# Optimization experiments

Hardware: AMD Instinct MI355X
Metric: run time of the kernel (lower is better)

## Reference

```python
import jax, jax.numpy as jnp
import numpy as np

BN_EPS = 1e-3
EPS = 1e-8
IGNORE = -1


def _head(x, w1, b1, g, be, w2, b2):
    # Linear -> BatchNorm1d (training: batch stats, biased var) -> ReLU -> Linear
    h = x @ w1 + b1
    mu = h.mean(axis=0)
    var = h.var(axis=0)  # biased, matches torch BN normalization
    h = (h - mu) * jax.lax.rsqrt(var + BN_EPS) * g + be
    h = jax.nn.relu(h)
    return h @ w2 + b2


def _bias_losses(a, b, mask):
    # faithful to compute_loss(bias_gt, bias_pred, mask); l1 and cosine are symmetric
    dist = jnp.sum(jnp.abs(a - b), axis=-1)
    denom = jnp.sum(mask) + EPS
    l1 = jnp.sum(dist * mask) / denom
    an = a / (jnp.linalg.norm(a, axis=-1, keepdims=True) + EPS)
    bn = b / (jnp.linalg.norm(b, axis=-1, keepdims=True) + EPS)
    cos = -jnp.sum(an * bn, axis=-1)
    cl = jnp.sum(cos * mask) / denom
    return l1, cl


def setup_inputs() -> dict:
    key = jax.random.key(0)
    ks = jax.random.split(key, 12)
    N, C, S = 1048576, 64, 20
    inp = {
        'feat': jax.random.normal(ks[0], (N, C), jnp.float32),
        'coord': jax.random.normal(ks[1], (N, 3), jnp.float32) * 2.0,
        'segment': jax.random.randint(ks[2], (N,), -1, S).astype(jnp.int32),
        'instance': jax.random.randint(ks[3], (N,), -1, 200).astype(jnp.int32),
        'instance_centroid': jax.random.normal(ks[4], (N, 3), jnp.float32) * 2.0,
        'w1_xy': jax.random.normal(ks[5], (C, C), jnp.float32) * 0.05,
        'b1_xy': jnp.zeros((C,), jnp.float32),
        'g_xy': jnp.ones((C,), jnp.float32),
        'be_xy': jnp.zeros((C,), jnp.float32),
        'w2_xy': jax.random.normal(ks[6], (C, 2), jnp.float32) * 0.05,
        'b2_xy': jnp.zeros((2,), jnp.float32),
        'w1_z': jax.random.normal(ks[7], (C, C), jnp.float32) * 0.05,
        'b1_z': jnp.zeros((C,), jnp.float32),
        'g_z': jnp.ones((C,), jnp.float32),
        'be_z': jnp.zeros((C,), jnp.float32),
        'w2_z': jax.random.normal(ks[8], (C, 1), jnp.float32) * 0.05,
        'b2_z': jnp.zeros((1,), jnp.float32),
        'w_seg': jax.random.normal(ks[9], (C, S), jnp.float32) * 0.05,
        'b_seg': jnp.zeros((S,), jnp.float32),
    }
    return inp


def reference(feat, coord, segment, instance, instance_centroid,
              w1_xy, b1_xy, g_xy, be_xy, w2_xy, b2_xy,
              w1_z, b1_z, g_z, be_z, w2_z, b2_z,
              w_seg, b_seg):
    bias_pred_xy = _head(feat, w1_xy, b1_xy, g_xy, be_xy, w2_xy, b2_xy)  # [N,2]
    bias_pred_z = _head(feat, w1_z, b1_z, g_z, be_z, w2_z, b2_z)         # [N,1]
    logit_pred = feat @ w_seg + b_seg                                     # [N,S]

    # cross-entropy with ignore_index=-1, unit class weights
    valid = (segment != IGNORE)
    tgt = jnp.where(valid, segment, 0)
    logp = jax.nn.log_softmax(logit_pred, axis=-1)
    nll = -jnp.take_along_axis(logp, tgt[:, None], axis=1)[:, 0]
    vf = valid.astype(logit_pred.dtype)
    seg_loss = jnp.sum(nll * vf) / jnp.sum(vf)

    mask = (instance != IGNORE).astype(feat.dtype)
    bias_gt = instance_centroid - coord
    l1_xy, cos_xy = _bias_losses(bias_gt[:, :2], bias_pred_xy, mask)
    l1_z, cos_z = _bias_losses(bias_gt[:, 2:3], bias_pred_z, mask)

    # faithful to original (bias_xy_l1 counted twice, xy cosine unused in total)
    loss = seg_loss + l1_xy + l1_xy + 0.5 * (l1_z + cos_z)
    return (loss, seg_loss, l1_xy, cos_xy, l1_z, cos_z)
```

## Files before the change

### kernel.cpp

```cpp
#include <hip/hip_runtime.h>
#include <hip/hip_bf16.h>

#define OFF_COLSUM 0
#define OFF_S      64
#define OFF_ACC    4160
#define OFF_DONE   4168
#define OFF_ZEND   4169
#define OFF_SHX    4176
#define OFF_SHZ    4240
#define OFF_W1XS   4304
#define OFF_W1ZS   6352
#define OFF_WSEGS  8400

typedef __attribute__((ext_vector_type(8))) short bf16x8;
typedef __attribute__((ext_vector_type(4))) float f32x4;

__device__ __forceinline__ unsigned short f2bfh(float x) {
    __hip_bfloat16 h = __float2bfloat16(x);
    return *reinterpret_cast<unsigned short*>(&h);
}

union BF8 { bf16x8 v; unsigned short u[8]; };

__device__ __forceinline__ void gload_lds16(const void* g, void* l) {
    __builtin_amdgcn_global_load_lds((const __attribute__((address_space(1))) void*)g,
                                     (__attribute__((address_space(3))) void*)l, 16, 0, 0);
}


__global__ __launch_bounds__(256, 2) void k_stats(const float* __restrict__ feat,
                                                  int N, int ntiles, int tpb,
                                                  float* __restrict__ ws) {
    __shared__ __align__(16) float ftile[2][4096];
    const int t = threadIdx.x;
    const int lane = t & 63, l15 = lane & 15, grp = lane >> 4, wv = t >> 6;

    const f32x4 z4 = {0.f, 0.f, 0.f, 0.f};
    f32x4 acc[4] = {z4, z4, z4, z4};
    float csum = 0.f;

    const int l3 = l15 & 3;
    const int cb_base = l15 >> 2;
    const int g1x8 = (grp & 1) * 8;

    const int ti0 = blockIdx.x * tpb;
    const int tiend = min(ti0 + tpb, ntiles);

    auto stage = [&](int bufi, int ti) {
        const int row0 = ti * 64;
        if (row0 + 64 <= N) {
#pragma unroll
            for (int c = 0; c < 4; c++) {
                const int r = (wv * 4 + c) * 4 + grp;
                const int u = l15 ^ (r & 15);
                gload_lds16(&feat[(size_t)(row0 + r) * 64 + u * 4],
                            &ftile[bufi][(wv * 4 + c) * 256]);
            }
        } else {
#pragma unroll
            for (int u2 = 0; u2 < 4; u2++) {
                const int i = t + u2 * 256;
                const int r = i >> 4, u = (i & 15) ^ (r & 15);
                float4 v = make_float4(0.f, 0.f, 0.f, 0.f);
                if (row0 + r < N) v = *(const float4*)&feat[(size_t)(row0 + r) * 64 + u * 4];
                *(float4*)&ftile[bufi][i * 4] = v;
            }
        }
    };

    if (ti0 < tiend) stage(0, ti0);
    int cur = 0;
    for (int ti = ti0; ti < tiend; ++ti) {
        __syncthreads();
        if (ti + 1 < tiend) stage(cur ^ 1, ti + 1);
        const float* fb = ftile[cur];

        bf16x8 fr[4][2];
#pragma unroll
        for (int s = 0; s < 4; s++) {
            const int g = (wv + s) & 3;
            const int cb = (g * 4 + cb_base) ^ g1x8;
#pragma unroll
            for (int h = 0; h < 2; h++) {
                const int pbase = h * 32 + grp * 8;
                float vs[8];
#pragma unroll
                for (int kk = 0; kk < 8; kk++)
                    vs[kk] = fb[(pbase + kk) * 64 + ((cb ^ kk) << 2) + l3];
                BF8 fv;
#pragma unroll
                for (int kk = 0; kk < 8; kk++) fv.u[kk] = f2bfh(vs[kk]);
                fr[s][h] = fv.v;
                if (s == 0) {
#pragma unroll
                    for (int kk = 0; kk < 8; kk++) csum += vs[kk];
                }
            }
        }
#pragma unroll
        for (int s = 0; s < 4; s++) {
            acc[s] = __builtin_amdgcn_mfma_f32_16x16x32_bf16(fr[0][0], fr[s][0], acc[s], 0, 0, 0);
            acc[s] = __builtin_amdgcn_mfma_f32_16x16x32_bf16(fr[0][1], fr[s][1], acc[s], 0, 0, 0);
        }
        cur ^= 1;
    }

    float* S = ws + OFF_S;
#pragma unroll
    for (int s = 0; s < 4; s++) {
        const int gj = (wv + s) & 3;
#pragma unroll
        for (int r = 0; r < 4; r++)
            atomicAdd(&S[(wv * 16 + grp * 4 + r) * 64 + gj * 16 + l15], acc[s][r]);
    }
    csum += __shfl_xor(csum, 16);
    csum += __shfl_xor(csum, 32);
    if (grp == 0) atomicAdd(&ws[OFF_COLSUM + wv * 16 + l15], csum);
}

__global__ __launch_bounds__(256) void k_prep(
    const float* __restrict__ w1xy, const float* __restrict__ b1xy,
    const float* __restrict__ gxy,  const float* __restrict__ bexy,
    const float* __restrict__ w1z,  const float* __restrict__ b1z,
    const float* __restrict__ gz,   const float* __restrict__ bez,
    const float* __restrict__ wseg, float Nf, float* __restrict__ ws) {
    __shared__ float S[64][64];
    __shared__ float cs[64];
    const int t = threadIdx.x;

    for (int i = t; i < 4096; i += 256) ((float*)S)[i] = ws[OFF_S + i];
    if (t < 64) cs[t] = ws[OFF_COLSUM + t];
    __syncthreads();

    if (t < 128) {
        const int head = t >> 6, j = t & 63;
        const float* w1 = head ? w1z : w1xy;
        float w[64];
#pragma unroll
        for (int k = 0; k < 64; k++) w[k] = w1[k * 64 + j];
        float d = 0.f;
#pragma unroll
        for (int k = 0; k < 64; k++) d = fmaf(cs[k], w[k], d);
        float quad = 0.f;
#pragma unroll
        for (int k = 0; k < 64; k++) {
            float rd = 0.f;
#pragma unroll
            for (int l = 0; l < 64; l++) rd = fmaf(S[k][l], w[l], rd);
            quad = fmaf(w[k], rd, quad);
        }
        const float b1 = head ? b1z[j] : b1xy[j];
        const float mu  = d / Nf + b1;
        const float eh2 = quad / Nf + 2.f * b1 * d / Nf + b1 * b1;
        const float var = eh2 - mu * mu;
        const float g  = head ? gz[j]  : gxy[j];
        const float be = head ? bez[j] : bexy[j];
        const float sc = g * rsqrtf(var + 1e-3f);
        const float sh = be - mu * sc;
        ws[(head ? OFF_SHZ : OFF_SHX) + j] = sh;
        unsigned short* dst = (unsigned short*)(ws + (head ? OFF_W1ZS : OFF_W1XS));
#pragma unroll
        for (int k = 0; k < 64; k++) dst[j * 64 + k] = f2bfh(w[k] * sc);
    } else if (t < 160) {
        const int j = t - 128;
        unsigned short* dst = (unsigned short*)(ws + OFF_WSEGS);
        for (int k = 0; k < 64; k++)
            dst[j * 64 + k] = (j < 20) ? f2bfh(wseg[k * 20 + j]) : (unsigned short)0;
    }
}

__global__ __launch_bounds__(256, 2) void k_loss(
    const float* __restrict__ feat, const float* __restrict__ coord,
    const int* __restrict__ seg, const int* __restrict__ inst,
    const float* __restrict__ cent,
    const unsigned short* __restrict__ w1xs, const unsigned short* __restrict__ w1zs,
    const unsigned short* __restrict__ wsegs,
    const float* __restrict__ shxv, const float* __restrict__ shzv,
    const float* __restrict__ w2xy, const float* __restrict__ b2xy,
    const float* __restrict__ w2z,  const float* __restrict__ b2z,
    const float* __restrict__ bseg,
    int N, int ntiles, int tpb, float* __restrict__ acc, float* __restrict__ out) {
    __shared__ __align__(16) float ftile[2][4096];
    __shared__ float red[4][8];

    const int t = threadIdx.x;
    const int lane = t & 63, l15 = lane & 15, grp = lane >> 4, wv = t >> 6;

    bf16x8 ax[4][2], az[4][2], ag[2][2];
#pragma unroll
    for (int nt = 0; nt < 4; nt++)
#pragma unroll
        for (int h = 0; h < 2; h++) {
            ax[nt][h] = *(const bf16x8*)&w1xs[(nt * 16 + l15) * 64 + grp * 8 + h * 32];
            az[nt][h] = *(const bf16x8*)&w1zs[(nt * 16 + l15) * 64 + grp * 8 + h * 32];
        }
#pragma unroll
    for (int nt = 0; nt < 2; nt++)
#pragma unroll
        for (int h = 0; h < 2; h++)
            ag[nt][h] = *(const bf16x8*)&wsegs[(nt * 16 + l15) * 64 + grp * 8 + h * 32];

    float shx_c[4][4], shz_c[4][4], w20[4][4], w21[4][4], w2zc[4][4], bs_c[2][4];
#pragma unroll
    for (int nt = 0; nt < 4; nt++)
#pragma unroll
        for (int r = 0; r < 4; r++) {
            const int c = nt * 16 + grp * 4 + r;
            shx_c[nt][r] = shxv[c]; shz_c[nt][r] = shzv[c];
            w20[nt][r] = w2xy[c * 2]; w21[nt][r] = w2xy[c * 2 + 1];
            w2zc[nt][r] = w2z[c];
        }
#pragma unroll
    for (int nt = 0; nt < 2; nt++)
#pragma unroll
        for (int r = 0; r < 4; r++) {
            const int c = nt * 16 + grp * 4 + r;
            bs_c[nt][r] = (c < 20) ? bseg[c] : -1e30f;
        }
    const float pb0 = b2xy[0], pb1 = b2xy[1], pbz = b2z[0];

    float s_nll = 0.f, s_vf = 0.f, s_l1xy = 0.f, s_cosxy = 0.f;
    float s_l1z = 0.f, s_cosz = 0.f, s_mask = 0.f;

    const int ti0 = blockIdx.x * tpb;
    const int tiend = min(ti0 + tpb, ntiles);

    auto stage = [&](int bufi, int ti) {
        const int row0 = ti * 64;
        if (row0 + 64 <= N) {
#pragma unroll
            for (int c = 0; c < 4; c++) {
                const int r = (wv * 4 + c) * 4 + grp;
                const int u = l15 ^ (r & 15);
                gload_lds16(&feat[(size_t)(row0 + r) * 64 + u * 4],
                            &ftile[bufi][(wv * 4 + c) * 256]);
            }
        } else {
#pragma unroll
            for (int u2 = 0; u2 < 4; u2++) {
                const int i = t + u2 * 256;
                const int r = i >> 4, u = (i & 15) ^ (r & 15);
                float4 v = make_float4(0.f, 0.f, 0.f, 0.f);
                if (row0 + r < N) v = *(const float4*)&feat[(size_t)(row0 + r) * 64 + u * 4];
                *(float4*)&ftile[bufi][i * 4] = v;
            }
        }
    };

    int p_tg = -1, p_iv = -1;
    float p_c0 = 0.f, p_c1 = 0.f, p_c2 = 0.f, p_e0 = 0.f, p_e1 = 0.f, p_e2 = 0.f;
    auto ptload = [&](int ti) {
        const int gp = ti * 64 + wv * 16 + l15;
        const bool inb = (gp < N);
        p_tg = inb ? seg[gp] : -1;
        p_iv = inb ? inst[gp] : -1;
        if (inb) {
            p_c0 = coord[(size_t)gp * 3]; p_c1 = coord[(size_t)gp * 3 + 1]; p_c2 = coord[(size_t)gp * 3 + 2];
            p_e0 = cent[(size_t)gp * 3];  p_e1 = cent[(size_t)gp * 3 + 1];  p_e2 = cent[(size_t)gp * 3 + 2];
        } else {
            p_c0 = p_c1 = p_c2 = p_e0 = p_e1 = p_e2 = 0.f;
        }
    };

    if (ti0 < tiend) { stage(0, ti0); ptload(ti0); }
    int cur = 0;
    for (int ti = ti0; ti < tiend; ++ti) {
        const int tg = p_tg, iv = p_iv;
        const float c0 = p_c0, c1 = p_c1, c2 = p_c2, e0 = p_e0, e1 = p_e1, e2 = p_e2;

        __syncthreads();
        if (ti + 1 < tiend) { stage(cur ^ 1, ti + 1); ptload(ti + 1); }

        const int p = wv * 16 + l15;
        const float* fb = ftile[cur];
        const float4 q0 = *(const float4*)&fb[(p * 16 + ((grp * 2)     ^ l15)) * 4];
        const float4 q1 = *(const float4*)&fb[(p * 16 + ((grp * 2 + 1) ^ l15)) * 4];
        const float4 q2 = *(const float4*)&fb[(p * 16 + ((8 + grp * 2) ^ l15)) * 4];
        const float4 q3 = *(const float4*)&fb[(p * 16 + ((9 + grp * 2) ^ l15)) * 4];
        BF8 b0, b1;
        b0.u[0] = f2bfh(q0.x); b0.u[1] = f2bfh(q0.y); b0.u[2] = f2bfh(q0.z); b0.u[3] = f2bfh(q0.w);
        b0.u[4] = f2bfh(q1.x); b0.u[5] = f2bfh(q1.y); b0.u[6] = f2bfh(q1.z); b0.u[7] = f2bfh(q1.w);
        b1.u[0] = f2bfh(q2.x); b1.u[1] = f2bfh(q2.y); b1.u[2] = f2bfh(q2.z); b1.u[3] = f2bfh(q2.w);
        b1.u[4] = f2bfh(q3.x); b1.u[5] = f2bfh(q3.y); b1.u[6] = f2bfh(q3.z); b1.u[7] = f2bfh(q3.w);

        f32x4 cg0 = {bs_c[0][0], bs_c[0][1], bs_c[0][2], bs_c[0][3]};
        cg0 = __builtin_amdgcn_mfma_f32_16x16x32_bf16(ag[0][0], b0.v, cg0, 0, 0, 0);
        cg0 = __builtin_amdgcn_mfma_f32_16x16x32_bf16(ag[0][1], b1.v, cg0, 0, 0, 0);
        f32x4 cg1 = {bs_c[1][0], bs_c[1][1], bs_c[1][2], bs_c[1][3]};
        cg1 = __builtin_amdgcn_mfma_f32_16x16x32_bf16(ag[1][0], b0.v, cg1, 0, 0, 0);
        cg1 = __builtin_amdgcn_mfma_f32_16x16x32_bf16(ag[1][1], b1.v, cg1, 0, 0, 0);
        float lmax = cg0[0];
#pragma unroll
        for (int r = 1; r < 4; r++) lmax = fmaxf(lmax, cg0[r]);
#pragma unroll
        for (int r = 0; r < 4; r++) lmax = fmaxf(lmax, cg1[r]);
        lmax = fmaxf(lmax, __shfl_xor(lmax, 16));
        lmax = fmaxf(lmax, __shfl_xor(lmax, 32));
        float se = 0.f;
#pragma unroll
        for (int r = 0; r < 4; r++) se += __expf(cg0[r] - lmax);
#pragma unroll
        for (int r = 0; r < 4; r++) se += __expf(cg1[r] - lmax);
        se += __shfl_xor(se, 16); se += __shfl_xor(se, 32);
        const float lse = lmax + __logf(se);
        float lt = 0.f;
#pragma unroll
        for (int r = 0; r < 4; r++) lt += (grp * 4 + r == tg) ? cg0[r] : 0.f;
#pragma unroll
        for (int r = 0; r < 4; r++) lt += (16 + grp * 4 + r == tg) ? cg1[r] : 0.f;
        lt += __shfl_xor(lt, 16); lt += __shfl_xor(lt, 32);
        const float vf = (tg >= 0) ? 1.f : 0.f;
        s_nll += (lse - lt) * vf;
        s_vf += vf;

        float s0 = 0.f, s1 = 0.f, szv = 0.f;
#pragma unroll
        for (int nt = 0; nt < 4; nt++) {
            f32x4 cc = {shx_c[nt][0], shx_c[nt][1], shx_c[nt][2], shx_c[nt][3]};
            cc = __builtin_amdgcn_mfma_f32_16x16x32_bf16(ax[nt][0], b0.v, cc, 0, 0, 0);
            cc = __builtin_amdgcn_mfma_f32_16x16x32_bf16(ax[nt][1], b1.v, cc, 0, 0, 0);
#pragma unroll
            for (int r = 0; r < 4; r++) {
                const float hx = fmaxf(cc[r], 0.f);
                s0 = fmaf(hx, w20[nt][r], s0);
                s1 = fmaf(hx, w21[nt][r], s1);
            }
            f32x4 cz = {shz_c[nt][0], shz_c[nt][1], shz_c[nt][2], shz_c[nt][3]};
            cz = __builtin_amdgcn_mfma_f32_16x16x32_bf16(az[nt][0], b0.v, cz, 0, 0, 0);
            cz = __builtin_amdgcn_mfma_f32_16x16x32_bf16(az[nt][1], b1.v, cz, 0, 0, 0);
#pragma unroll
            for (int r = 0; r < 4; r++) {
                const float hz = fmaxf(cz[r], 0.f);
                szv = fmaf(hz, w2zc[nt][r], szv);
            }
        }
        s0 += __shfl_xor(s0, 16);  s0 += __shfl_xor(s0, 32);
        s1 += __shfl_xor(s1, 16);  s1 += __shfl_xor(s1, 32);
        szv += __shfl_xor(szv, 16); szv += __shfl_xor(szv, 32);
        const float p0 = s0 + pb0, p1 = s1 + pb1, pz = szv + pbz;

        const float mk = (iv >= 0) ? 1.f : 0.f;
        const float a0 = e0 - c0, a1 = e1 - c1, a2 = e2 - c2;
        s_l1xy += (fabsf(a0 - p0) + fabsf(a1 - p1)) * mk;
        const float na = sqrtf(a0 * a0 + a1 * a1) + 1e-8f;
        const float nb = sqrtf(p0 * p0 + p1 * p1) + 1e-8f;
        s_cosxy -= ((a0 * p0 + a1 * p1) / (na * nb)) * mk;
        s_l1z += fabsf(a2 - pz) * mk;
        const float naz = fabsf(a2) + 1e-8f, nbz = fabsf(pz) + 1e-8f;
        s_cosz -= ((a2 * pz) / (naz * nbz)) * mk;
        s_mask += mk;

        cur ^= 1;
    }

    float v[7] = {s_nll * 0.25f, s_vf * 0.25f, s_l1xy * 0.25f, s_cosxy * 0.25f,
                  s_l1z * 0.25f, s_cosz * 0.25f, s_mask * 0.25f};
#pragma unroll
    for (int i = 0; i < 7; i++) {
#pragma unroll
        for (int o = 32; o > 0; o >>= 1) v[i] += __shfl_down(v[i], o);
    }
    if (lane == 0) {
#pragma unroll
        for (int i = 0; i < 7; i++) red[wv][i] = v[i];
    }
    __syncthreads();
    if (t < 7) {
        float s = red[0][t] + red[1][t] + red[2][t] + red[3][t];
        atomicAdd(&acc[t], s);
    }
    __syncthreads();
    if (t == 0) {
        __threadfence();
        int* done = (int*)(acc + (OFF_DONE - OFF_ACC));
        if (atomicAdd(done, 1) == (int)gridDim.x - 1) {
            __threadfence();
            float sv[7];
#pragma unroll
            for (int i = 0; i < 7; i++) sv[i] = atomicAdd(&acc[i], 0.f);
            const float segl = sv[0] / sv[1];
            const float den = sv[6] + 1e-8f;
            const float l1xy = sv[2] / den, cosxy = sv[3] / den;
            const float l1z = sv[4] / den, cosz = sv[5] / den;
            out[0] = segl + l1xy + l1xy + 0.5f * (l1z + cosz);
            out[1] = segl;
            out[2] = l1xy;
            out[3] = cosxy;
            out[4] = l1z;
            out[5] = cosz;
        }
    }
}

extern "C" void kernel_launch(void* const* d_in, const int* in_sizes, int n_in,
                              void* d_out, int out_size, void* d_ws, size_t ws_size,
                              hipStream_t stream) {
    const float* feat  = (const float*)d_in[0];
    const float* coord = (const float*)d_in[1];
    const int*   segm  = (const int*)d_in[2];
    const int*   inst  = (const int*)d_in[3];
    const float* cent  = (const float*)d_in[4];
    const float* w1xy  = (const float*)d_in[5];
    const float* b1xy  = (const float*)d_in[6];
    const float* gxy   = (const float*)d_in[7];
    const float* bexy  = (const float*)d_in[8];
    const float* w2xy  = (const float*)d_in[9];
    const float* b2xy  = (const float*)d_in[10];
    const float* w1z   = (const float*)d_in[11];
    const float* b1z   = (const float*)d_in[12];
    const float* gz    = (const float*)d_in[13];
    const float* bez   = (const float*)d_in[14];
    const float* w2z   = (const float*)d_in[15];
    const float* b2z   = (const float*)d_in[16];
    const float* wseg  = (const float*)d_in[17];
    const float* bseg  = (const float*)d_in[18];

    const int N = in_sizes[0] / 64;
    float* ws = (float*)d_ws;
    const int ntiles = (N + 63) >> 6;

    const int grid_s = 512;
    const int tpb_s = (ntiles + grid_s - 1) / grid_s;
    const int grid_l = 512;
    const int tpb_l = (ntiles + grid_l - 1) / grid_l;

    hipMemsetAsync(d_ws, 0, OFF_ZEND * sizeof(float), stream);

    k_stats<<<grid_s, 256, 0, stream>>>(feat, N, ntiles, tpb_s, ws);
    k_prep<<<1, 256, 0, stream>>>(w1xy, b1xy, gxy, bexy, w1z, b1z, gz, bez, wseg,
                                  (float)N, ws);
    k_loss<<<grid_l, 256, 0, stream>>>(
        feat, coord, segm, inst, cent,
        (const unsigned short*)(ws + OFF_W1XS),
        (const unsigned short*)(ws + OFF_W1ZS),
        (const unsigned short*)(ws + OFF_WSEGS),
        ws + OFF_SHX, ws + OFF_SHZ,
        w2xy, b2xy, w2z, b2z, bseg, N, ntiles, tpb_l,
        ws + OFF_ACC, (float*)d_out);
}
```

Baseline: 188.9 us.

## Stage feat tile via registers as transposed bf16 in LDS for stats GEMM

The Gram/column-sum kernel now loads feat rows into registers, converts them to bf16 once, and writes a transposed, swizzled, packed bf16 tile to LDS. The MFMA fragments then come from single 16-byte LDS reads instead of eight scalar fp32 reads plus conversions per fragment. This replaces async global_load_lds double buffering with register prefetch and a single LDS buffer that needs two barriers per tile. It cuts LDS traffic and conversion work, at the cost of less overlap between memory and compute and more register pressure.

```diff
diff --git a/kernel.cpp b/kernel.cpp
--- a/kernel.cpp
+++ b/kernel.cpp
@@ -27,82 +27,81 @@
                                      (__attribute__((address_space(3))) void*)l, 16, 0, 0);
 }
 
-
 __global__ __launch_bounds__(256, 2) void k_stats(const float* __restrict__ feat,
                                                   int N, int ntiles, int tpb,
                                                   float* __restrict__ ws) {
-    __shared__ __align__(16) float ftile[2][4096];
+    __shared__ __align__(16) unsigned int bt[64 * 36];
     const int t = threadIdx.x;
     const int lane = t & 63, l15 = lane & 15, grp = lane >> 4, wv = t >> 6;
+    const int q = t & 15;
+    const int pp = t >> 4;
 
     const f32x4 z4 = {0.f, 0.f, 0.f, 0.f};
     f32x4 acc[4] = {z4, z4, z4, z4};
-    float csum = 0.f;
-
-    const int l3 = l15 & 3;
-    const int cb_base = l15 >> 2;
-    const int g1x8 = (grp & 1) * 8;
+    float cs4[4] = {0.f, 0.f, 0.f, 0.f};
+
+    const int sw_w = 4 * (q & 7);
+    int woff[4][2];
+#pragma unroll
+    for (int c = 0; c < 4; c++) {
+        woff[c][0] = (4 * q + c) * 36 + (pp ^ sw_w);
+        woff[c][1] = (4 * q + c) * 36 + ((pp + 16) ^ sw_w);
+    }
+    int roff[4][2];
+#pragma unroll
+    for (int s = 0; s < 4; s++) {
+        const int g = (wv + s) & 3;
+        const int ch = g * 16 + l15;
+        const int sw = 4 * ((ch >> 2) & 7);
+#pragma unroll
+        for (int h = 0; h < 2; h++)
+            roff[s][h] = ch * 72 + 2 * ((h * 16 + grp * 4) ^ sw);
+    }
 
     const int ti0 = blockIdx.x * tpb;
     const int tiend = min(ti0 + tpb, ntiles);
 
-    auto stage = [&](int bufi, int ti) {
-        const int row0 = ti * 64;
-        if (row0 + 64 <= N) {
-#pragma unroll
-            for (int c = 0; c < 4; c++) {
-                const int r = (wv * 4 + c) * 4 + grp;
-                const int u = l15 ^ (r & 15);
-                gload_lds16(&feat[(size_t)(row0 + r) * 64 + u * 4],
-                            &ftile[bufi][(wv * 4 + c) * 256]);
-            }
-        } else {
-#pragma unroll
-            for (int u2 = 0; u2 < 4; u2++) {
-                const int i = t + u2 * 256;
-                const int r = i >> 4, u = (i & 15) ^ (r & 15);
-                float4 v = make_float4(0.f, 0.f, 0.f, 0.f);
-                if (row0 + r < N) v = *(const float4*)&feat[(size_t)(row0 + r) * 64 + u * 4];
-                *(float4*)&ftile[bufi][i * 4] = v;
-            }
-        }
+    float4 fA0, fA1, fB0, fB1;
+    auto gload = [&](int ti) {
+        const int p0 = ti * 64 + 2 * pp;
+        const int pB = p0 + 32;
+        fA0 = make_float4(0.f, 0.f, 0.f, 0.f); fA1 = fA0; fB0 = fA0; fB1 = fA0;
+        if (p0 < N)     fA0 = *(const float4*)&feat[(size_t)p0 * 64 + q * 4];
+        if (p0 + 1 < N) fA1 = *(const float4*)&feat[(size_t)(p0 + 1) * 64 + q * 4];
+        if (pB < N)     fB0 = *(const float4*)&feat[(size_t)pB * 64 + q * 4];
+        if (pB + 1 < N) fB1 = *(const float4*)&feat[(size_t)(pB + 1) * 64 + q * 4];
     };
-
-    if (ti0 < tiend) stage(0, ti0);
-    int cur = 0;
+    auto commit = [&]() {
+        const float a0[4] = {fA0.x, fA0.y, fA0.z, fA0.w};
+        const float a1[4] = {fA1.x, fA1.y, fA1.z, fA1.w};
+        const float b0[4] = {fB0.x, fB0.y, fB0.z, fB0.w};
+        const float b1[4] = {fB1.x, fB1.y, fB1.z, fB1.w};
+#pragma unroll
+        for (int c = 0; c < 4; c++) {
+            cs4[c] += a0[c] + a1[c] + b0[c] + b1[c];
+            bt[woff[c][0]] = (unsigned)f2bfh(a0[c]) | ((unsigned)f2bfh(a1[c]) << 16);
+            bt[woff[c][1]] = (unsigned)f2bfh(b0[c]) | ((unsigned)f2bfh(b1[c]) << 16);
+        }
+    };
+
+    if (ti0 < tiend) gload(ti0);
     for (int ti = ti0; ti < tiend; ++ti) {
+        commit();
         __syncthreads();
-        if (ti + 1 < tiend) stage(cur ^ 1, ti + 1);
-        const float* fb = ftile[cur];
-
+        if (ti + 1 < tiend) gload(ti + 1);
+        const unsigned short* bu = (const unsigned short*)bt;
         bf16x8 fr[4][2];
 #pragma unroll
-        for (int s = 0; s < 4; s++) {
-            const int g = (wv + s) & 3;
-            const int cb = (g * 4 + cb_base) ^ g1x8;
-#pragma unroll
-            for (int h = 0; h < 2; h++) {
-                const int pbase = h * 32 + grp * 8;
-                float vs[8];
-#pragma unroll
-                for (int kk = 0; kk < 8; kk++)
-                    vs[kk] = fb[(pbase + kk) * 64 + ((cb ^ kk) << 2) + l3];
-                BF8 fv;
-#pragma unroll
-                for (int kk = 0; kk < 8; kk++) fv.u[kk] = f2bfh(vs[kk]);
-                fr[s][h] = fv.v;
-                if (s == 0) {
-#pragma unroll
-                    for (int kk = 0; kk < 8; kk++) csum += vs[kk];
-                }
-            }
-        }
+        for (int s = 0; s < 4; s++)
+#pragma unroll
+            for (int h = 0; h < 2; h++)
+                fr[s][h] = *(const bf16x8*)&bu[roff[s][h]];
 #pragma unroll
         for (int s = 0; s < 4; s++) {
             acc[s] = __builtin_amdgcn_mfma_f32_16x16x32_bf16(fr[0][0], fr[s][0], acc[s], 0, 0, 0);
             acc[s] = __builtin_amdgcn_mfma_f32_16x16x32_bf16(fr[0][1], fr[s][1], acc[s], 0, 0, 0);
         }
-        cur ^= 1;
+        __syncthreads();
     }
 
     float* S = ws + OFF_S;
@@ -113,9 +112,12 @@
         for (int r = 0; r < 4; r++)
             atomicAdd(&S[(wv * 16 + grp * 4 + r) * 64 + gj * 16 + l15], acc[s][r]);
     }
-    csum += __shfl_xor(csum, 16);
-    csum += __shfl_xor(csum, 32);
-    if (grp == 0) atomicAdd(&ws[OFF_COLSUM + wv * 16 + l15], csum);
+#pragma unroll
+    for (int c = 0; c < 4; c++) {
+        float v = cs4[c];
+        v += __shfl_xor(v, 16); v += __shfl_xor(v, 32);
+        if (grp == 0) atomicAdd(&ws[OFF_COLSUM + 4 * q + c], v);
+    }
 }
 
 __global__ __launch_bounds__(256) void k_prep(
```

Measured after the change: 373.6 us. 97.8% more time.
